# Kernel optimization log

Hardware: AMD Instinct MI355X
Metric: run time of the kernel (lower is better)

Reference implementation:

```python
import jax, jax.numpy as jnp
import numpy as np

DIM = 2048
NUM_HEADS = 4  # hardcoded in RetNext.__init__
HEAD_DIM = DIM // NUM_HEADS
B, T = 4, 4096


def setup_inputs() -> dict:
    key = jax.random.key(0)
    ks = jax.random.split(key, 7)
    s = 1.0 / np.sqrt(DIM)  # roughly nn.Linear init scale
    return {
        "x": jax.random.normal(ks[0], (B, T, DIM), dtype=jnp.float32),
        "Wk": jax.random.normal(ks[1], (DIM, DIM), dtype=jnp.float32) * s,
        "bk": jax.random.normal(ks[2], (DIM,), dtype=jnp.float32) * s,
        "Wq": jax.random.normal(ks[3], (DIM, DIM), dtype=jnp.float32) * s,
        "bq": jax.random.normal(ks[4], (DIM,), dtype=jnp.float32) * s,
        "Wv": jax.random.normal(ks[5], (DIM, DIM), dtype=jnp.float32) * s,
        "bv": jax.random.normal(ks[6], (DIM,), dtype=jnp.float32) * s,
    }


def reference(x, Wk, bk, Wq, bq, Wv, bv):
    bsz, seq_len, _ = x.shape
    # nn.Linear: y = x @ W.T + b
    k = x @ Wk.T + bk
    q = x @ Wq.T + bq
    v = x @ Wv.T + bv
    # (b, s, h, d) -> (b, h, s, d)
    k = k.reshape(bsz, seq_len, NUM_HEADS, HEAD_DIM).transpose(0, 2, 1, 3)
    q = q.reshape(bsz, seq_len, NUM_HEADS, HEAD_DIM).transpose(0, 2, 1, 3)
    v = v.reshape(bsz, seq_len, NUM_HEADS, HEAD_DIM).transpose(0, 2, 1, 3)
    # states = k^T @ v : (b, h, d, d)
    states = jnp.einsum("bhsd,bhse->bhde", k, v)
    # out = q @ states : (b, h, s, d) -- returned WITHOUT reshape, as in the source
    out = jnp.einsum("bhsd,bhde->bhse", q, states)
    return out
```

## Files before the change

### kernel.cpp

```cpp
#include <hip/hip_runtime.h>
#include <cstdint>
#include <cstddef>

typedef __bf16 bf16;
typedef bf16 bf16x8 __attribute__((ext_vector_type(8)));
typedef float f32x4 __attribute__((ext_vector_type(4)));
typedef unsigned short u16;
typedef u16 u16x4 __attribute__((ext_vector_type(4)));
typedef u16 u16x8 __attribute__((ext_vector_type(8)));

__device__ __forceinline__ u16 f2bf(float f) {
    uint32_t u = __builtin_bit_cast(uint32_t, f);
    u += 0x7FFFu + ((u >> 16) & 1u);
    return (u16)(u >> 16);
}

#define AS1C(p) ((const __attribute__((address_space(1))) uint32_t*)(p))
#define AS3(p)  ((__attribute__((address_space(3))) uint32_t*)(p))

__device__ __forceinline__ void gemm_core(const bf16* __restrict__ Ablk,
                                          const bf16* __restrict__ Btblk,
                                          int lda, int ldb, int K,
                                          f32x4 acc[4][4])
{
    __shared__ bf16 lA[4096];
    __shared__ bf16 lB[4096];

    const int tid  = threadIdx.x;
    const int wave = tid >> 6;
    const int lane = tid & 63;
    const int lrow = lane >> 2;
    const int kcol = (lane & 3) << 3;

    const bf16* ga0 = Ablk  + (size_t)(wave * 32 + lrow) * lda + kcol;
    const bf16* ga1 = ga0 + (size_t)16 * lda;
    const bf16* gb0 = Btblk + (size_t)(wave * 32 + lrow) * ldb + kcol;
    const bf16* gb1 = gb0 + (size_t)16 * ldb;
    bf16* la0 = &lA[wave * 1024];
    bf16* la1 = &lA[wave * 1024 + 512];
    bf16* lb0 = &lB[wave * 1024];
    bf16* lb1 = &lB[wave * 1024 + 512];

    const int wm    = (wave >> 1) * 64;
    const int wn    = (wave & 1) * 64;
    const int col16 = lane & 15;
    const int quad  = lane >> 4;
    const bf16* pa = &lA[(wm + col16) * 32 + quad * 8];
    const bf16* pb = &lB[(wn + col16) * 32 + quad * 8];

    for (int kb = 0; kb < K; kb += 32) {
        __builtin_amdgcn_global_load_lds(AS1C(ga0 + kb), AS3(la0), 16, 0, 0);
        __builtin_amdgcn_global_load_lds(AS1C(ga1 + kb), AS3(la1), 16, 0, 0);
        __builtin_amdgcn_global_load_lds(AS1C(gb0 + kb), AS3(lb0), 16, 0, 0);
        __builtin_amdgcn_global_load_lds(AS1C(gb1 + kb), AS3(lb1), 16, 0, 0);
        __syncthreads();

        bf16x8 av[4], bv[4];
        #pragma unroll
        for (int i = 0; i < 4; ++i) av[i] = *(const bf16x8*)(pa + i * 512);
        #pragma unroll
        for (int i = 0; i < 4; ++i) bv[i] = *(const bf16x8*)(pb + i * 512);

        #pragma unroll
        for (int mi = 0; mi < 4; ++mi)
            #pragma unroll
            for (int ni = 0; ni < 4; ++ni)
                acc[mi][ni] = __builtin_amdgcn_mfma_f32_16x16x32_bf16(
                    av[mi], bv[ni], acc[mi][ni], 0, 0, 0);
        __syncthreads();
    }
}

__global__ __launch_bounds__(256) void cast_bf16(const float* __restrict__ src,
                                                 u16* __restrict__ dst, int n8)
{
    int i = blockIdx.x * 256 + threadIdx.x;
    if (i >= n8) return;
    const float4* s = (const float4*)src + (size_t)i * 2;
    float4 f0 = s[0], f1 = s[1];
    u16x8 o;
    o[0] = f2bf(f0.x); o[1] = f2bf(f0.y); o[2] = f2bf(f0.z); o[3] = f2bf(f0.w);
    o[4] = f2bf(f1.x); o[5] = f2bf(f1.y); o[6] = f2bf(f1.z); o[7] = f2bf(f1.w);
    *((u16x8*)dst + i) = o;
}

__global__ __launch_bounds__(256) void gemm_qkv(
    const bf16* __restrict__ xb,
    const bf16* __restrict__ Wkb, const bf16* __restrict__ Wqb, const bf16* __restrict__ Wvb,
    const float* __restrict__ bk, const float* __restrict__ bq, const float* __restrict__ bv,
    u16* __restrict__ qout, u16* __restrict__ kT, u16* __restrict__ vT)
{
    const int bx = blockIdx.x;
    const int by = blockIdx.y;
    const int region = by >> 4;
    const int nloc = (by & 15) << 7;

    const bf16* W     = (region == 0) ? Wkb : (region == 1) ? Wqb : Wvb;
    const float* bias = (region == 0) ? bk  : (region == 1) ? bq  : bv;

    f32x4 acc[4][4] = {};
    gemm_core(xb + (size_t)bx * 128 * 2048, W + (size_t)nloc * 2048,
              2048, 2048, 2048, acc);

    const int lane = threadIdx.x & 63, wave = threadIdx.x >> 6;
    const int wm = (wave >> 1) * 64, wn = (wave & 1) * 64;
    const int col16 = lane & 15, quad = lane >> 4;

    if (region == 1) {
        #pragma unroll
        for (int mi = 0; mi < 4; ++mi) {
            int row = bx * 128 + wm + mi * 16 + quad * 4;
            #pragma unroll
            for (int ni = 0; ni < 4; ++ni) {
                int col = nloc + wn + ni * 16 + col16;
                float b = bias[col];
                #pragma unroll
                for (int r = 0; r < 4; ++r)
                    qout[(size_t)(row + r) * 2048 + col] = f2bf(acc[mi][ni][r] + b);
            }
        }
    } else {
        u16* T = (region == 0) ? kT : vT;
        const int b_ = bx >> 5;
        const int h_ = nloc >> 9;
        const int bh = b_ * 4 + h_;
        #pragma unroll
        for (int mi = 0; mi < 4; ++mi) {
            int s = ((bx & 31) * 128) + wm + mi * 16 + quad * 4;
            #pragma unroll
            for (int ni = 0; ni < 4; ++ni) {
                int fcol = nloc + wn + ni * 16 + col16;
                int d = fcol & 511;
                float b = bias[fcol];
                u16x4 p;
                #pragma unroll
                for (int r = 0; r < 4; ++r) p[r] = f2bf(acc[mi][ni][r] + b);
                *(u16x4*)&T[((size_t)(bh * 512 + d)) * 4096 + s] = p;
            }
        }
    }
}

__global__ __launch_bounds__(256) void gemm_states(
    const u16* __restrict__ vT, const u16* __restrict__ kT, u16* __restrict__ ST)
{
    const int bh = blockIdx.z;
    const int m0 = blockIdx.x * 128;
    const int n0 = blockIdx.y * 128;

    f32x4 acc[4][4] = {};
    gemm_core((const bf16*)vT + (size_t)bh * 2097152 + (size_t)m0 * 4096,
              (const bf16*)kT + (size_t)bh * 2097152 + (size_t)n0 * 4096,
              4096, 4096, 4096, acc);

    const int lane = threadIdx.x & 63, wave = threadIdx.x >> 6;
    const int wm = (wave >> 1) * 64, wn = (wave & 1) * 64;
    const int col16 = lane & 15, quad = lane >> 4;
    #pragma unroll
    for (int mi = 0; mi < 4; ++mi) {
        int row = m0 + wm + mi * 16 + quad * 4;
        #pragma unroll
        for (int ni = 0; ni < 4; ++ni) {
            int col = n0 + wn + ni * 16 + col16;
            #pragma unroll
            for (int r = 0; r < 4; ++r)
                ST[(size_t)bh * 262144 + (size_t)(row + r) * 512 + col] =
                    f2bf(acc[mi][ni][r]);
        }
    }
}

__global__ __launch_bounds__(256) void gemm_out(
    const u16* __restrict__ qb, const u16* __restrict__ ST, float* __restrict__ out)
{
    const int bh = blockIdx.z;
    const int b_ = bh >> 2, h_ = bh & 3;
    const int m0 = blockIdx.x * 128;
    const int n0 = blockIdx.y * 128;

    f32x4 acc[4][4] = {};
    gemm_core((const bf16*)qb + ((size_t)(b_ * 4096 + m0)) * 2048 + h_ * 512,
              (const bf16*)ST + (size_t)bh * 262144 + (size_t)n0 * 512,
              2048, 512, 512, acc);

    const int lane = threadIdx.x & 63, wave = threadIdx.x >> 6;
    const int wm = (wave >> 1) * 64, wn = (wave & 1) * 64;
    const int col16 = lane & 15, quad = lane >> 4;
    #pragma unroll
    for (int mi = 0; mi < 4; ++mi) {
        int row = m0 + wm + mi * 16 + quad * 4;
        #pragma unroll
        for (int ni = 0; ni < 4; ++ni) {
            int col = n0 + wn + ni * 16 + col16;
            #pragma unroll
            for (int r = 0; r < 4; ++r)
                out[(size_t)bh * 2097152 + (size_t)(row + r) * 512 + col] =
                    acc[mi][ni][r];
        }
    }
}

extern "C" void kernel_launch(void* const* d_in, const int* in_sizes, int n_in,
                              void* d_out, int out_size, void* d_ws, size_t ws_size,
                              hipStream_t stream)
{
    (void)in_sizes; (void)n_in; (void)out_size; (void)ws_size;
    const float* x  = (const float*)d_in[0];
    const float* Wk = (const float*)d_in[1];
    const float* bk = (const float*)d_in[2];
    const float* Wq = (const float*)d_in[3];
    const float* bq = (const float*)d_in[4];
    const float* Wv = (const float*)d_in[5];
    const float* bv = (const float*)d_in[6];
    float* out = (float*)d_out;

    u16* ws  = (u16*)d_ws;
    u16* xb  = ws;
    u16* Wkb = ws  + 33554432;
    u16* Wqb = Wkb + 4194304;
    u16* Wvb = Wqb + 4194304;
    u16* qb  = Wvb + 4194304;
    u16* kT  = qb  + 33554432;
    u16* vT  = kT  + 33554432;
    u16* ST  = vT  + 33554432;

    cast_bf16<<<16384, 256, 0, stream>>>(x,  xb,  4194304);
    cast_bf16<<<2048,  256, 0, stream>>>(Wk, Wkb, 524288);
    cast_bf16<<<2048,  256, 0, stream>>>(Wq, Wqb, 524288);
    cast_bf16<<<2048,  256, 0, stream>>>(Wv, Wvb, 524288);

    gemm_qkv<<<dim3(128, 48), 256, 0, stream>>>(
        (const bf16*)xb, (const bf16*)Wkb, (const bf16*)Wqb, (const bf16*)Wvb,
        bk, bq, bv, qb, kT, vT);

    gemm_states<<<dim3(4, 4, 16), 256, 0, stream>>>(vT, kT, ST);

    gemm_out<<<dim3(32, 4, 16), 256, 0, stream>>>(qb, ST, out);
}
```

Before: 982.0 us.

## Split-K the states GEMM with atomic fp32 accumulation and swap QKV grid order

The states GEMM (K=4096) previously launched only 256 blocks, which underfills the GPU. It now splits K into four chunks across blockIdx.z, atomically accumulates into a zeroed fp32 buffer that reuses the x-bf16 workspace, and converts to bf16 in a new kernel. The QKV GEMM grid is also transposed so consecutive blocks share the same x row tile and walk across weight columns, which changes cache reuse. The cost is a memset, fp32 atomics and an extra conversion pass, plus non-deterministic summation order.

```diff
diff --git a/kernel.cpp b/kernel.cpp
--- a/kernel.cpp
+++ b/kernel.cpp
@@ -84,14 +84,27 @@
     *((u16x8*)dst + i) = o;
 }
 
+__global__ __launch_bounds__(256) void st_cvt(const float* __restrict__ src,
+                                              u16* __restrict__ dst, int n8)
+{
+    int i = blockIdx.x * 256 + threadIdx.x;
+    if (i >= n8) return;
+    const float4* s = (const float4*)src + (size_t)i * 2;
+    float4 f0 = s[0], f1 = s[1];
+    u16x8 o;
+    o[0] = f2bf(f0.x); o[1] = f2bf(f0.y); o[2] = f2bf(f0.z); o[3] = f2bf(f0.w);
+    o[4] = f2bf(f1.x); o[5] = f2bf(f1.y); o[6] = f2bf(f1.z); o[7] = f2bf(f1.w);
+    *((u16x8*)dst + i) = o;
+}
+
 __global__ __launch_bounds__(256) void gemm_qkv(
     const bf16* __restrict__ xb,
     const bf16* __restrict__ Wkb, const bf16* __restrict__ Wqb, const bf16* __restrict__ Wvb,
     const float* __restrict__ bk, const float* __restrict__ bq, const float* __restrict__ bv,
     u16* __restrict__ qout, u16* __restrict__ kT, u16* __restrict__ vT)
 {
-    const int bx = blockIdx.x;
-    const int by = blockIdx.y;
+    const int by = blockIdx.x;
+    const int bx = blockIdx.y;
     const int region = by >> 4;
     const int nloc = (by & 15) << 7;
 
@@ -142,16 +155,17 @@
 }
 
 __global__ __launch_bounds__(256) void gemm_states(
-    const u16* __restrict__ vT, const u16* __restrict__ kT, u16* __restrict__ ST)
-{
-    const int bh = blockIdx.z;
+    const u16* __restrict__ vT, const u16* __restrict__ kT, float* __restrict__ STf)
+{
+    const int bh = blockIdx.z >> 2;
+    const int kc = blockIdx.z & 3;
     const int m0 = blockIdx.x * 128;
     const int n0 = blockIdx.y * 128;
 
     f32x4 acc[4][4] = {};
-    gemm_core((const bf16*)vT + (size_t)bh * 2097152 + (size_t)m0 * 4096,
-              (const bf16*)kT + (size_t)bh * 2097152 + (size_t)n0 * 4096,
-              4096, 4096, 4096, acc);
+    gemm_core((const bf16*)vT + (size_t)bh * 2097152 + (size_t)m0 * 4096 + kc * 1024,
+              (const bf16*)kT + (size_t)bh * 2097152 + (size_t)n0 * 4096 + kc * 1024,
+              4096, 4096, 1024, acc);
 
     const int lane = threadIdx.x & 63, wave = threadIdx.x >> 6;
     const int wm = (wave >> 1) * 64, wn = (wave & 1) * 64;
@@ -164,8 +178,8 @@
             int col = n0 + wn + ni * 16 + col16;
             #pragma unroll
             for (int r = 0; r < 4; ++r)
-                ST[(size_t)bh * 262144 + (size_t)(row + r) * 512 + col] =
-                    f2bf(acc[mi][ni][r]);
+                atomicAdd(&STf[(size_t)bh * 262144 + (size_t)(row + r) * 512 + col],
+                          acc[mi][ni][r]);
         }
     }
 }
@@ -223,17 +237,22 @@
     u16* kT  = qb  + 33554432;
     u16* vT  = kT  + 33554432;
     u16* ST  = vT  + 33554432;
+    float* STf = (float*)xb;
 
     cast_bf16<<<16384, 256, 0, stream>>>(x,  xb,  4194304);
     cast_bf16<<<2048,  256, 0, stream>>>(Wk, Wkb, 524288);
     cast_bf16<<<2048,  256, 0, stream>>>(Wq, Wqb, 524288);
     cast_bf16<<<2048,  256, 0, stream>>>(Wv, Wvb, 524288);
 
-    gemm_qkv<<<dim3(128, 48), 256, 0, stream>>>(
+    gemm_qkv<<<dim3(48, 128), 256, 0, stream>>>(
         (const bf16*)xb, (const bf16*)Wkb, (const bf16*)Wqb, (const bf16*)Wvb,
         bk, bq, bv, qb, kT, vT);
 
-    gemm_states<<<dim3(4, 4, 16), 256, 0, stream>>>(vT, kT, ST);
+    hipMemsetAsync(STf, 0, (size_t)16 * 512 * 512 * 4, stream);
+
+    gemm_states<<<dim3(4, 4, 64), 256, 0, stream>>>(vT, kT, STf);
+
+    st_cvt<<<2048, 256, 0, stream>>>(STf, ST, 524288);
 
     gemm_out<<<dim3(32, 4, 16), 256, 0, stream>>>(qb, ST, out);
 }
```

New measurement: 1.028 ms. +4.7%, slower.
